# Optimization experiments

Hardware: AMD Instinct MI355X
Metric: run time of the kernel (lower is better)

## Reference

```python
import jax, jax.numpy as jnp
import numpy as np

B, L, D = 2, 2048, 2048
H, HKV, HD = 32, 8, 64
EPS = 1e-5
THETA = 1000000.0


def rms_norm(x, w):
    # normalize over last dim (head_dim)
    return x * jax.lax.rsqrt(jnp.mean(x * x, axis=-1, keepdims=True) + EPS) * w


def apply_rope(t):
    # t: (B, heads, L, HD); non-traditional (half-split) RoPE, offset=0
    half = HD // 2
    inv_freq = THETA ** (-jnp.arange(0, HD, 2, dtype=jnp.float32) / HD)  # (half,)
    ang = jnp.arange(L, dtype=jnp.float32)[:, None] * inv_freq           # (L, half)
    cos, sin = jnp.cos(ang), jnp.sin(ang)
    x1, x2 = t[..., :half], t[..., half:]
    return jnp.concatenate([x1 * cos - x2 * sin, x2 * cos + x1 * sin], axis=-1)


def setup_inputs() -> dict:
    key = jax.random.key(0)
    ks = jax.random.split(key, 5)
    s = 0.02
    return {
        "x": jax.random.normal(ks[0], (B, L, D), dtype=jnp.float32),
        "Wq": jax.random.normal(ks[1], (D, H * HD), dtype=jnp.float32) * s,
        "Wk": jax.random.normal(ks[2], (D, HKV * HD), dtype=jnp.float32) * s,
        "Wv": jax.random.normal(ks[3], (D, HKV * HD), dtype=jnp.float32) * s,
        "Wo": jax.random.normal(ks[4], (H * HD, D), dtype=jnp.float32) * s,
        "q_norm_w": jnp.ones((HD,), dtype=jnp.float32),
        "k_norm_w": jnp.ones((HD,), dtype=jnp.float32),
    }


def reference(x, Wq, Wk, Wv, Wo, q_norm_w, k_norm_w):
    scale = HD ** -0.5
    g = H // HKV  # GQA group size
    # projections
    q = (x @ Wq).reshape(B, L, H, HD)
    k = (x @ Wk).reshape(B, L, HKV, HD)
    v = (x @ Wv).reshape(B, L, HKV, HD)
    # per-head RMSNorm, then to (B, heads, L, HD)
    q = jnp.transpose(rms_norm(q, q_norm_w), (0, 2, 1, 3))
    k = jnp.transpose(rms_norm(k, k_norm_w), (0, 2, 1, 3))
    v = jnp.transpose(v, (0, 2, 1, 3))
    # RoPE
    q = apply_rope(q)
    k = apply_rope(k)
    # grouped-query attention with causal mask
    qg = q.reshape(B, HKV, g, L, HD)
    scores = jnp.einsum('bhgqd,bhkd->bhgqk', qg, k) * scale  # (B,HKV,g,L,L)
    causal = jnp.tril(jnp.ones((L, L), dtype=bool))
    scores = jnp.where(causal, scores, jnp.finfo(scores.dtype).min)
    probs = jax.nn.softmax(scores, axis=-1)
    out = jnp.einsum('bhgqk,bhkd->bhgqd', probs, v)           # (B,HKV,g,L,HD)
    out = jnp.transpose(out.reshape(B, H, L, HD), (0, 2, 1, 3)).reshape(B, L, H * HD)
    return out @ Wo
```

## Files before the change

### kernel.cpp

```cpp
#include <hip/hip_runtime.h>
#include <math.h>
#include <stdint.h>

#define B_ 2
#define L_ 2048
#define D_ 2048
#define H_ 32
#define HKV_ 8
#define HD_ 64
#define EPS_ 1e-5f

typedef _Float16 half_t;
typedef __attribute__((ext_vector_type(8))) _Float16 half8_t;
typedef __attribute__((ext_vector_type(4))) _Float16 half4_t;
typedef __attribute__((ext_vector_type(4))) float float4_t;

typedef const __attribute__((address_space(1))) uint32_t glb_u32;
typedef __attribute__((address_space(3))) uint32_t lds_u32;
#define GLOAD_LDS16(gp, lp) \
  __builtin_amdgcn_global_load_lds((glb_u32*)(gp), (lds_u32*)(lp), 16, 0, 0)

__device__ __forceinline__ float4_t fmax4(float4_t a, float4_t b) {
  float4_t r;
  r[0] = fmaxf(a[0], b[0]); r[1] = fmaxf(a[1], b[1]);
  r[2] = fmaxf(a[2], b[2]); r[3] = fmaxf(a[3], b[3]);
  return r;
}

__device__ __forceinline__ uint32_t pk_f16(float a, float b) {
  auto p = __builtin_amdgcn_cvt_pkrtz(a, b);
  return __builtin_bit_cast(uint32_t, p);
}

__global__ __launch_bounds__(256) void prep_all(
    const float* __restrict__ x,
    const float* __restrict__ Wq, const float* __restrict__ Wk,
    const float* __restrict__ Wv, const float* __restrict__ Wo,
    half_t* __restrict__ xh,
    half_t* __restrict__ Wqt, half_t* __restrict__ Wkt,
    half_t* __restrict__ Wvt, half_t* __restrict__ Wot)
{
  __shared__ float tile[64][65];
  const int t = threadIdx.x;
  int id = blockIdx.x;

  if (id < 4096) {
    size_t i = ((size_t)id * 256 + t) * 8;
    float4 v0 = *(const float4*)&x[i];
    float4 v1 = *(const float4*)&x[i + 4];
    half8_t h;
    h[0] = (half_t)v0.x; h[1] = (half_t)v0.y; h[2] = (half_t)v0.z; h[3] = (half_t)v0.w;
    h[4] = (half_t)v1.x; h[5] = (half_t)v1.y; h[6] = (half_t)v1.z; h[7] = (half_t)v1.w;
    *(half8_t*)&xh[i] = h;
    return;
  }
  id -= 4096;
  const float* W; half_t* Wt; int N;
  if (id < 1024)      { W = Wq; Wt = Wqt; N = 2048; }
  else if (id < 1280) { id -= 1024; W = Wk; Wt = Wkt; N = 512; }
  else if (id < 1536) { id -= 1280; W = Wv; Wt = Wvt; N = 512; }
  else                { id -= 1536; W = Wo; Wt = Wot; N = 2048; }
  const int K = 2048;
  int tk = id & 31, tn = id >> 5;
  int k0 = tk * 64, n0 = tn * 64;

  int rr = t >> 6, cc = t & 63;
#pragma unroll
  for (int i = 0; i < 16; i++)
    tile[rr + i * 4][cc] = W[(size_t)(k0 + rr + i * 4) * N + n0 + cc];
  __syncthreads();

  int rn = t >> 2, q4 = (t & 3) * 16;
  half8_t h0, h1;
#pragma unroll
  for (int u = 0; u < 8; u++) h0[u] = (half_t)tile[q4 + u][rn];
#pragma unroll
  for (int u = 0; u < 8; u++) h1[u] = (half_t)tile[q4 + 8 + u][rn];
  *(half8_t*)&Wt[(size_t)(n0 + rn) * K + k0 + q4]     = h0;
  *(half8_t*)&Wt[(size_t)(n0 + rn) * K + k0 + q4 + 8] = h1;
}

template <typename CT>
__device__ __forceinline__ void gemm_tile_f16(
    const half_t* __restrict__ A, const half_t* __restrict__ Bt,
    CT* __restrict__ C, int K, int ldc, int row0, int col0,
    bool tv, half_t* __restrict__ vtp)
{
  __shared__ __align__(16) half_t As[2][128 * 32];
  __shared__ __align__(16) half_t Bs[2][128 * 32];
  const int t    = threadIdx.x;
  const int lane = t & 63;
  const int w    = t >> 6;
  const int quad = lane >> 4, c = lane & 15;
  const int wm = (w >> 1) * 64, wn = (w & 1) * 64;

  float4_t acc[4][4];
#pragma unroll
  for (int i = 0; i < 4; i++)
#pragma unroll
    for (int j = 0; j < 4; j++) acc[i][j] = (float4_t){0.f, 0.f, 0.f, 0.f};

  const int srow = w * 32 + (lane >> 2);
  const int scol = (lane & 3) * 8;
  const half_t* Ag0 = A  + (size_t)(row0 + srow) * K + scol;
  const half_t* Ag1 = Ag0 + (size_t)16 * K;
  const half_t* Bg0 = Bt + (size_t)(col0 + srow) * K + scol;
  const half_t* Bg1 = Bg0 + (size_t)16 * K;
  const int wb0 = (w * 32) * 32;
  const int wb1 = (w * 32 + 16) * 32;

  GLOAD_LDS16(Ag0, &As[0][wb0]);
  GLOAD_LDS16(Ag1, &As[0][wb1]);
  GLOAD_LDS16(Bg0, &Bs[0][wb0]);
  GLOAD_LDS16(Bg1, &Bs[0][wb1]);
  __syncthreads();

  int cur = 0;
  for (int k0 = 0; k0 < K; k0 += 32) {
    if (k0 + 32 < K) {
      GLOAD_LDS16(Ag0 + k0 + 32, &As[cur ^ 1][wb0]);
      GLOAD_LDS16(Ag1 + k0 + 32, &As[cur ^ 1][wb1]);
      GLOAD_LDS16(Bg0 + k0 + 32, &Bs[cur ^ 1][wb0]);
      GLOAD_LDS16(Bg1 + k0 + 32, &Bs[cur ^ 1][wb1]);
    }

    half8_t af[4], bf[4];
#pragma unroll
    for (int i = 0; i < 4; i++)
      af[i] = *(const half8_t*)&As[cur][(wm + i * 16 + c) * 32 + quad * 8];
#pragma unroll
    for (int j = 0; j < 4; j++)
      bf[j] = *(const half8_t*)&Bs[cur][(wn + j * 16 + c) * 32 + quad * 8];
#pragma unroll
    for (int i = 0; i < 4; i++)
#pragma unroll
      for (int j = 0; j < 4; j++)
        acc[i][j] = __builtin_amdgcn_mfma_f32_16x16x32_f16(af[i], bf[j], acc[i][j], 0, 0, 0);

    __syncthreads();
    cur ^= 1;
  }

  if (tv) {
    const int kvq = (col0 + wn) >> 6;
#pragma unroll
    for (int i = 0; i < 4; i++) {
      int row = row0 + wm + i * 16 + quad * 4;
      int bb  = row >> 11;
      int tok = row & (L_ - 1);
      half_t* vbase = vtp + (((size_t)bb * HKV_ + kvq) * HD_ + c) * L_ + tok;
#pragma unroll
      for (int j = 0; j < 4; j++) {
        half4_t h4;
#pragma unroll
        for (int r = 0; r < 4; r++) h4[r] = (half_t)acc[i][j][r];
        *(half4_t*)(vbase + (size_t)(j * 16) * L_) = h4;
      }
    }
  } else {
#pragma unroll
    for (int i = 0; i < 4; i++)
#pragma unroll
      for (int r = 0; r < 4; r++) {
        CT* Cp = C + (size_t)(row0 + wm + i * 16 + quad * 4 + r) * ldc + col0 + wn + c;
#pragma unroll
        for (int j = 0; j < 4; j++)
          Cp[j * 16] = (CT)acc[i][j][r];
      }
  }
}

__global__ __launch_bounds__(256) void qkv_gemm_h(
    const half_t* __restrict__ xh,
    const half_t* __restrict__ Wqt, const half_t* __restrict__ Wkt,
    const half_t* __restrict__ Wvt,
    half_t* __restrict__ qh, half_t* __restrict__ kh, half_t* __restrict__ vt)
{
  int lin = (int)blockIdx.y * 24 + (int)blockIdx.x;
  int xcd = lin & 7, idx = lin >> 3;
  int cy = xcd >> 2, cx = xcd & 3;
  int by = cy * 16 + idx / 6;
  int bx = cx * 6 + idx % 6;

  const half_t* Bt; half_t* C; int ldc, col0; bool tv = false;
  if (bx < 16)      { Bt = Wqt; C = qh; ldc = H_ * HD_;   col0 = bx * 128; }
  else if (bx < 20) { Bt = Wkt; C = kh; ldc = HKV_ * HD_; col0 = (bx - 16) * 128; }
  else              { Bt = Wvt; C = vt; ldc = HKV_ * HD_; col0 = (bx - 20) * 128;
                      tv = true; }
  gemm_tile_f16<half_t>(xh, Bt, C, D_, ldc, by * 128, col0, tv, vt);
}

__global__ __launch_bounds__(256) void out_gemm_h(
    const half_t* __restrict__ attn, const half_t* __restrict__ Wot,
    float* __restrict__ out)
{
  int lin = (int)blockIdx.y * 16 + (int)blockIdx.x;
  int xcd = lin & 7, idx = lin >> 3;
  int cy = xcd >> 1, cx = xcd & 1;
  int by = cy * 8 + idx / 8;
  int bx = cx * 8 + idx % 8;
  gemm_tile_f16<float>(attn, Wot, out, H_ * HD_, D_, by * 128, bx * 128,
                       false, nullptr);
}

__device__ __forceinline__ void norm_rope_row(
    half_t* __restrict__ buf, float wv, int row, int nheads, int lognh,
    int lane, float oscale, float cv, float sv)
{
  int head  = row & (nheads - 1);
  int token = row >> lognh;

  size_t idx = (size_t)token * (nheads * HD_) + head * HD_ + lane;
  float x = (float)buf[idx];

  float ss = x * x;
#pragma unroll
  for (int off = 32; off; off >>= 1) ss += __shfl_xor(ss, off);
  float xn = x * rsqrtf(ss * (1.0f / HD_) + EPS_) * wv;

  float partner = __shfl_xor(xn, 32);
  float res = (lane < 32) ? (xn * cv - partner * sv) : (xn * cv + partner * sv);
  buf[idx] = (half_t)(res * oscale);
}

__global__ __launch_bounds__(256) void mid(
    half_t* __restrict__ kh, const float* __restrict__ kw,
    float* __restrict__ ct, float* __restrict__ st)
{
  const int t = threadIdx.x;
  int id = blockIdx.x;

  if (id < 256) {
    int e = id * 256 + t;
    int l = e >> 5, fi = e & 31;
    float inv_freq = exp2f((float)fi * -0.622862853f);
    float ang = (float)l * inv_freq;
    ct[e] = cosf(ang);
    st[e] = sinf(ang);
    return;
  }
  id -= 256;
  const int lane = t & 63;
  const int wv   = t >> 6;
  int fi = lane & 31;
  float inv_freq = exp2f((float)fi * -0.622862853f);
  int row0  = (id * 4 + wv) * 4;
  int token = row0 >> 3;
  int l     = token & (L_ - 1);
  float ang = (float)l * inv_freq;
  float cvv = cosf(ang), svv = sinf(ang);
  float wk  = kw[lane];
#pragma unroll
  for (int u = 0; u < 4; u++)
    norm_rope_row(kh, wk, row0 + u, HKV_, 3, lane, 1.0f, cvv, svv);
}

__global__ __launch_bounds__(512) void flash_mfma2(
    const half_t* __restrict__ Qh, const half_t* __restrict__ Kh,
    const half_t* __restrict__ Vt, half_t* __restrict__ Oa,
    const float* __restrict__ qw,
    const float* __restrict__ ct, const float* __restrict__ st)
{
  __shared__ __align__(16) half_t Ks[64][72];
  __shared__ __align__(16) half_t Vs[64][72];
  __shared__ __align__(16) half_t Ps[128][72];
  __shared__ __align__(16) float  Ab[128];

  const int t    = threadIdx.x;
  const int w    = t >> 6;
  const int lane = t & 63;
  const int quad = lane >> 4;
  const int c    = lane & 15;
  const int h = blockIdx.y, b = blockIdx.z;
  const int kvh = h >> 2;

  const half_t* kbase = Kh + (size_t)(b * L_) * (HKV_ * HD_) + kvh * HD_;
  const half_t* vbase = Vt + (size_t)((b * HKV_ + kvh) * HD_) * L_;
  const int sr = t >> 3;
  const int su = (t & 7) * 8;

  half8_t ones;
#pragma unroll
  for (int u = 0; u < 8; u++) ones[u] = (half_t)1.0f;

  for (int pass = 0; pass < 2; pass++) {
    const int qb  = pass ? (15 - (int)blockIdx.x) : (int)blockIdx.x;
    const int q0  = qb * 128;
    const int wq0 = q0 + w * 16;

    half8_t qf0, qf1;
    {
      const half_t* qp = Qh + ((size_t)(b * L_ + wq0 + c)) * (H_ * HD_) + h * HD_;
      half8_t r0 = *(const half8_t*)&qp[quad * 8];
      half8_t r1 = *(const half8_t*)&qp[32 + quad * 8];
      float x1[8], x2[8];
      float ss = 0.f;
#pragma unroll
      for (int j = 0; j < 8; j++) {
        x1[j] = (float)r0[j]; x2[j] = (float)r1[j];
        ss += x1[j] * x1[j] + x2[j] * x2[j];
      }
      ss += __shfl_xor(ss, 16);
      ss += __shfl_xor(ss, 32);
      float rn = rsqrtf(ss * (1.0f / HD_) + EPS_);
      const int l = wq0 + c;
      float4 c0 = *(const float4*)&ct[l * 32 + quad * 8];
      float4 c1 = *(const float4*)&ct[l * 32 + quad * 8 + 4];
      float4 s0 = *(const float4*)&st[l * 32 + quad * 8];
      float4 s1 = *(const float4*)&st[l * 32 + quad * 8 + 4];
      float4 w0 = *(const float4*)&qw[quad * 8];
      float4 w1 = *(const float4*)&qw[quad * 8 + 4];
      float4 w2 = *(const float4*)&qw[32 + quad * 8];
      float4 w3 = *(const float4*)&qw[32 + quad * 8 + 4];
      const float cs[8] = {c0.x, c0.y, c0.z, c0.w, c1.x, c1.y, c1.z, c1.w};
      const float sn[8] = {s0.x, s0.y, s0.z, s0.w, s1.x, s1.y, s1.z, s1.w};
      const float wa[8] = {w0.x, w0.y, w0.z, w0.w, w1.x, w1.y, w1.z, w1.w};
      const float wb[8] = {w2.x, w2.y, w2.z, w2.w, w3.x, w3.y, w3.z, w3.w};
#pragma unroll
      for (int j = 0; j < 8; j++) {
        float xa = x1[j] * rn * wa[j];
        float xb = x2[j] * rn * wb[j];
        qf0[j] = (half_t)((xa * cs[j] - xb * sn[j]) * 0.180336880f);
        qf1[j] = (half_t)((xb * cs[j] + xa * sn[j]) * 0.180336880f);
      }
    }

    float4_t o[5];
#pragma unroll
    for (int dt = 0; dt < 5; dt++) o[dt] = (float4_t){0.f, 0.f, 0.f, 0.f};
    float mm = -__builtin_inff();

    half8_t kr, vr;
    kr = *(const half8_t*)(kbase + (size_t)sr * (HKV_ * HD_) + su);
    vr = *(const half8_t*)(vbase + (size_t)sr * L_ + su);

    const int last = (q0 + 127) >> 6;
    for (int kt = 0; kt <= last; kt++) {
      const int kk0 = kt * 64;
      __syncthreads();
      *(half8_t*)&Ks[sr][su] = kr;
      *(half8_t*)&Vs[sr][su] = vr;
      __syncthreads();
      if (kt < last) {
        kr = *(const half8_t*)(kbase + (size_t)(kk0 + 64 + sr) * (HKV_ * HD_) + su);
        vr = *(const half8_t*)(vbase + (size_t)sr * L_ + kk0 + 64 + su);
      }
      if (kk0 > wq0 + 15) continue;

      float4_t S[4];
      __builtin_amdgcn_s_setprio(1);
#pragma unroll
      for (int tt = 0; tt < 4; tt++) {
        half8_t kf0 = *(const half8_t*)&Ks[tt * 16 + c][quad * 8];
        half8_t kf1 = *(const half8_t*)&Ks[tt * 16 + c][32 + quad * 8];
        float4_t s = (float4_t){0.f, 0.f, 0.f, 0.f};
        s = __builtin_amdgcn_mfma_f32_16x16x32_f16(kf0, qf0, s, 0, 0, 0);
        s = __builtin_amdgcn_mfma_f32_16x16x32_f16(kf1, qf1, s, 0, 0, 0);
        S[tt] = s;
      }
      __builtin_amdgcn_s_setprio(0);

      if (kk0 + 63 > wq0) {
#pragma unroll
        for (int tt = 0; tt < 4; tt++) {
          int base = kk0 + tt * 16 + quad * 4 - (wq0 + c);
#pragma unroll
          for (int r = 0; r < 4; r++)
            if (base + r > 0) S[tt][r] = -__builtin_inff();
        }
      }

      {
        float4_t m4 = fmax4(fmax4(S[0], S[1]), fmax4(S[2], S[3]));
        float mloc = fmaxf(fmaxf(m4[0], m4[1]), fmaxf(m4[2], m4[3]));
        mloc = fmaxf(mloc, __shfl_xor(mloc, 16));
        mloc = fmaxf(mloc, __shfl_xor(mloc, 32));
        if (__any(mloc > mm + 8.0f)) {
          float mnew = fmaxf(mm, mloc);
          float al = exp2f(mm - mnew);
          mm = mnew;
          if (quad == 0) Ab[w * 16 + c] = al;
          float4_t av = *(const float4_t*)&Ab[w * 16 + quad * 4];
#pragma unroll
          for (int dt = 0; dt < 5; dt++)
#pragma unroll
            for (int r = 0; r < 4; r++) o[dt][r] *= av[r];
        }
#pragma unroll
        for (int tt = 0; tt < 4; tt++) {
#pragma unroll
          for (int r = 0; r < 4; r++) S[tt][r] = exp2f(S[tt][r] - mm);
          uint2 pw;
          pw.x = pk_f16(S[tt][0], S[tt][1]);
          pw.y = pk_f16(S[tt][2], S[tt][3]);
          *(uint2*)&Ps[w * 16 + c][tt * 16 + quad * 4] = pw;
        }
      }

      half8_t pf0 = *(const half8_t*)&Ps[w * 16 + c][quad * 8];
      half8_t pf1 = *(const half8_t*)&Ps[w * 16 + c][32 + quad * 8];
      __builtin_amdgcn_s_setprio(1);
      o[4] = __builtin_amdgcn_mfma_f32_16x16x32_f16(pf0, ones, o[4], 0, 0, 0);
      o[4] = __builtin_amdgcn_mfma_f32_16x16x32_f16(pf1, ones, o[4], 0, 0, 0);
#pragma unroll
      for (int dt = 0; dt < 4; dt++) {
        half8_t vf0 = *(const half8_t*)&Vs[dt * 16 + c][quad * 8];
        half8_t vf1 = *(const half8_t*)&Vs[dt * 16 + c][32 + quad * 8];
        o[dt] = __builtin_amdgcn_mfma_f32_16x16x32_f16(pf0, vf0, o[dt], 0, 0, 0);
        o[dt] = __builtin_amdgcn_mfma_f32_16x16x32_f16(pf1, vf1, o[dt], 0, 0, 0);
      }
      __builtin_amdgcn_s_setprio(0);
    }

#pragma unroll
    for (int r = 0; r < 4; r++) {
      float inv = 1.0f / o[4][r];
      half_t* op = Oa + ((size_t)(b * L_ + wq0 + quad * 4 + r)) * (H_ * HD_)
                 + h * HD_ + c;
#pragma unroll
      for (int dt = 0; dt < 4; dt++)
        op[dt * 16] = (half_t)(o[dt][r] * inv);
    }
  }
}

extern "C" void kernel_launch(void* const* d_in, const int* in_sizes, int n_in,
                              void* d_out, int out_size, void* d_ws, size_t ws_size,
                              hipStream_t stream)
{
  const float* x  = (const float*)d_in[0];
  const float* Wq = (const float*)d_in[1];
  const float* Wk = (const float*)d_in[2];
  const float* Wv = (const float*)d_in[3];
  const float* Wo = (const float*)d_in[4];
  const float* qw = (const float*)d_in[5];
  const float* kw = (const float*)d_in[6];
  float* out = (float*)d_out;

  const size_t XN = (size_t)B_ * L_ * D_;
  const size_t QN = (size_t)B_ * L_ * H_ * HD_;
  const size_t KN = (size_t)B_ * L_ * HKV_ * HD_;
  const size_t WQ = (size_t)D_ * H_ * HD_;
  const size_t WK = (size_t)D_ * HKV_ * HD_;

  half_t* p   = (half_t*)d_ws;
  half_t* xh  = p;  p += XN;
  half_t* Wqt = p;  p += WQ;
  half_t* Wkt = p;  p += WK;
  half_t* Wvt = p;  p += WK;
  half_t* Wot = p;  p += WQ;
  half_t* qh  = p;  p += QN;
  half_t* kh  = p;  p += KN;
  half_t* vt  = p;  p += KN;
  half_t* attn = xh;

  float* ct = (float*)Wqt;
  float* st = ct + 65536;

  prep_all<<<6656, 256, 0, stream>>>(x, Wq, Wk, Wv, Wo, xh, Wqt, Wkt, Wvt, Wot);

  qkv_gemm_h<<<dim3(24, 32), 256, 0, stream>>>(xh, Wqt, Wkt, Wvt, qh, kh, vt);

  mid<<<256 + 2048, 256, 0, stream>>>(kh, kw, ct, st);

  flash_mfma2<<<dim3(8, H_, B_), 512, 0, stream>>>(qh, kh, vt, attn, qw, ct, st);

  out_gemm_h<<<dim3(16, 32), 256, 0, stream>>>(attn, Wot, out);
}
```

Measured before the change: 315.3 us.

## Software-pipeline flash attention: overlap QK^T of next tile with softmax/PV of previous

Double-buffers the K and V shared-memory tiles and restructures the KV loop so the QK^T MFMAs for tile kt are issued before the softmax and PV step of tile kt-1. This lets matrix work overlap with the exp/max VALU work of the previous tile. The cost is twice the K/V LDS footprint, which may lower occupancy, and extra registers to hold the pending score tile. It also adds more control flow around the pending state.

```diff
diff --git a/kernel.cpp b/kernel.cpp
--- a/kernel.cpp
+++ b/kernel.cpp
@@ -261,8 +261,8 @@
     const float* __restrict__ qw,
     const float* __restrict__ ct, const float* __restrict__ st)
 {
-  __shared__ __align__(16) half_t Ks[64][72];
-  __shared__ __align__(16) half_t Vs[64][72];
+  __shared__ __align__(16) half_t Ks[2][64][72];
+  __shared__ __align__(16) half_t Vs[2][64][72];
   __shared__ __align__(16) half_t Ps[128][72];
   __shared__ __align__(16) float  Ab[128];
 
@@ -330,73 +330,31 @@
     for (int dt = 0; dt < 5; dt++) o[dt] = (float4_t){0.f, 0.f, 0.f, 0.f};
     float mm = -__builtin_inff();
 
-    half8_t kr, vr;
-    kr = *(const half8_t*)(kbase + (size_t)sr * (HKV_ * HD_) + su);
-    vr = *(const half8_t*)(vbase + (size_t)sr * L_ + su);
-
-    const int last = (q0 + 127) >> 6;
-    for (int kt = 0; kt <= last; kt++) {
-      const int kk0 = kt * 64;
-      __syncthreads();
-      *(half8_t*)&Ks[sr][su] = kr;
-      *(half8_t*)&Vs[sr][su] = vr;
-      __syncthreads();
-      if (kt < last) {
-        kr = *(const half8_t*)(kbase + (size_t)(kk0 + 64 + sr) * (HKV_ * HD_) + su);
-        vr = *(const half8_t*)(vbase + (size_t)sr * L_ + kk0 + 64 + su);
-      }
-      if (kk0 > wq0 + 15) continue;
-
-      float4_t S[4];
-      __builtin_amdgcn_s_setprio(1);
+    auto smpv = [&](float4_t S[4], int vsel) {
+      float4_t m4 = fmax4(fmax4(S[0], S[1]), fmax4(S[2], S[3]));
+      float mloc = fmaxf(fmaxf(m4[0], m4[1]), fmaxf(m4[2], m4[3]));
+      mloc = fmaxf(mloc, __shfl_xor(mloc, 16));
+      mloc = fmaxf(mloc, __shfl_xor(mloc, 32));
+      if (__any(mloc > mm + 8.0f)) {
+        float mnew = fmaxf(mm, mloc);
+        float al = exp2f(mm - mnew);
+        mm = mnew;
+        if (quad == 0) Ab[w * 16 + c] = al;
+        float4_t av = *(const float4_t*)&Ab[w * 16 + quad * 4];
+#pragma unroll
+        for (int dt = 0; dt < 5; dt++)
+#pragma unroll
+          for (int r = 0; r < 4; r++) o[dt][r] *= av[r];
+      }
 #pragma unroll
       for (int tt = 0; tt < 4; tt++) {
-        half8_t kf0 = *(const half8_t*)&Ks[tt * 16 + c][quad * 8];
-        half8_t kf1 = *(const half8_t*)&Ks[tt * 16 + c][32 + quad * 8];
-        float4_t s = (float4_t){0.f, 0.f, 0.f, 0.f};
-        s = __builtin_amdgcn_mfma_f32_16x16x32_f16(kf0, qf0, s, 0, 0, 0);
-        s = __builtin_amdgcn_mfma_f32_16x16x32_f16(kf1, qf1, s, 0, 0, 0);
-        S[tt] = s;
-      }
-      __builtin_amdgcn_s_setprio(0);
-
-      if (kk0 + 63 > wq0) {
-#pragma unroll
-        for (int tt = 0; tt < 4; tt++) {
-          int base = kk0 + tt * 16 + quad * 4 - (wq0 + c);
-#pragma unroll
-          for (int r = 0; r < 4; r++)
-            if (base + r > 0) S[tt][r] = -__builtin_inff();
-        }
-      }
-
-      {
-        float4_t m4 = fmax4(fmax4(S[0], S[1]), fmax4(S[2], S[3]));
-        float mloc = fmaxf(fmaxf(m4[0], m4[1]), fmaxf(m4[2], m4[3]));
-        mloc = fmaxf(mloc, __shfl_xor(mloc, 16));
-        mloc = fmaxf(mloc, __shfl_xor(mloc, 32));
-        if (__any(mloc > mm + 8.0f)) {
-          float mnew = fmaxf(mm, mloc);
-          float al = exp2f(mm - mnew);
-          mm = mnew;
-          if (quad == 0) Ab[w * 16 + c] = al;
-          float4_t av = *(const float4_t*)&Ab[w * 16 + quad * 4];
-#pragma unroll
-          for (int dt = 0; dt < 5; dt++)
-#pragma unroll
-            for (int r = 0; r < 4; r++) o[dt][r] *= av[r];
-        }
-#pragma unroll
-        for (int tt = 0; tt < 4; tt++) {
-#pragma unroll
-          for (int r = 0; r < 4; r++) S[tt][r] = exp2f(S[tt][r] - mm);
-          uint2 pw;
-          pw.x = pk_f16(S[tt][0], S[tt][1]);
-          pw.y = pk_f16(S[tt][2], S[tt][3]);
-          *(uint2*)&Ps[w * 16 + c][tt * 16 + quad * 4] = pw;
-        }
-      }
-
+#pragma unroll
+        for (int r = 0; r < 4; r++) S[tt][r] = exp2f(S[tt][r] - mm);
+        uint2 pw;
+        pw.x = pk_f16(S[tt][0], S[tt][1]);
+        pw.y = pk_f16(S[tt][2], S[tt][3]);
+        *(uint2*)&Ps[w * 16 + c][tt * 16 + quad * 4] = pw;
+      }
       half8_t pf0 = *(const half8_t*)&Ps[w * 16 + c][quad * 8];
       half8_t pf1 = *(const half8_t*)&Ps[w * 16 + c][32 + quad * 8];
       __builtin_amdgcn_s_setprio(1);
@@ -404,13 +362,69 @@
       o[4] = __builtin_amdgcn_mfma_f32_16x16x32_f16(pf1, ones, o[4], 0, 0, 0);
 #pragma unroll
       for (int dt = 0; dt < 4; dt++) {
-        half8_t vf0 = *(const half8_t*)&Vs[dt * 16 + c][quad * 8];
-        half8_t vf1 = *(const half8_t*)&Vs[dt * 16 + c][32 + quad * 8];
+        half8_t vf0 = *(const half8_t*)&Vs[vsel][dt * 16 + c][quad * 8];
+        half8_t vf1 = *(const half8_t*)&Vs[vsel][dt * 16 + c][32 + quad * 8];
         o[dt] = __builtin_amdgcn_mfma_f32_16x16x32_f16(pf0, vf0, o[dt], 0, 0, 0);
         o[dt] = __builtin_amdgcn_mfma_f32_16x16x32_f16(pf1, vf1, o[dt], 0, 0, 0);
       }
       __builtin_amdgcn_s_setprio(0);
+    };
+
+    half8_t kr, vr;
+    kr = *(const half8_t*)(kbase + (size_t)sr * (HKV_ * HD_) + su);
+    vr = *(const half8_t*)(vbase + (size_t)sr * L_ + su);
+
+    const int last = (q0 + 127) >> 6;
+    bool pend = false;
+    float4_t Sp[4];
+
+    for (int kt = 0; kt <= last; kt++) {
+      const int kk0 = kt * 64;
+      __syncthreads();
+      *(half8_t*)&Ks[kt & 1][sr][su] = kr;
+      *(half8_t*)&Vs[kt & 1][sr][su] = vr;
+      __syncthreads();
+      if (kt < last) {
+        kr = *(const half8_t*)(kbase + (size_t)(kk0 + 64 + sr) * (HKV_ * HD_) + su);
+        vr = *(const half8_t*)(vbase + (size_t)sr * L_ + kk0 + 64 + su);
+      }
+
+      const bool doit = (kk0 <= wq0 + 15);
+      float4_t Sc[4];
+      if (doit) {
+        __builtin_amdgcn_s_setprio(1);
+#pragma unroll
+        for (int tt = 0; tt < 4; tt++) {
+          half8_t kf0 = *(const half8_t*)&Ks[kt & 1][tt * 16 + c][quad * 8];
+          half8_t kf1 = *(const half8_t*)&Ks[kt & 1][tt * 16 + c][32 + quad * 8];
+          float4_t s = (float4_t){0.f, 0.f, 0.f, 0.f};
+          s = __builtin_amdgcn_mfma_f32_16x16x32_f16(kf0, qf0, s, 0, 0, 0);
+          s = __builtin_amdgcn_mfma_f32_16x16x32_f16(kf1, qf1, s, 0, 0, 0);
+          Sc[tt] = s;
+        }
+        __builtin_amdgcn_s_setprio(0);
+        if (kk0 + 63 > wq0) {
+#pragma unroll
+          for (int tt = 0; tt < 4; tt++) {
+            int base = kk0 + tt * 16 + quad * 4 - (wq0 + c);
+#pragma unroll
+            for (int r = 0; r < 4; r++)
+              if (base + r > 0) Sc[tt][r] = -__builtin_inff();
+          }
+        }
+      }
+
+      if (pend)
+        smpv(Sp, (kt - 1) & 1);
+
+      if (doit) {
+#pragma unroll
+        for (int tt = 0; tt < 4; tt++) Sp[tt] = Sc[tt];
+      }
+      pend = doit;
     }
+    if (pend)
+      smpv(Sp, last & 1);
 
 #pragma unroll
     for (int r = 0; r < 4; r++) {
```

After: 352.3 us. +11.8%, slower.
